# Kernel tuning notes

Hardware: AMD Instinct MI355X
Metric: run time of the kernel (lower is better)

Reference implementation:

```python
import jax, jax.numpy as jnp
import numpy as np

B, L, N, DOUT = 8, 8192, 256, 256  # batch, seq_len, state_dim, output_dim


def setup_inputs() -> dict:
    key = jax.random.key(0)
    k_u, k_h, k_w = jax.random.split(key, 3)
    u = jax.random.normal(k_u, (B, L, 1), dtype=jnp.float32)
    # impulse response buffer (stands in for A_bar^i @ B_bar rows); decay-scaled for realism
    h = jax.random.normal(k_h, (L, N), dtype=jnp.float32) * 0.02
    W = jax.random.normal(k_w, (DOUT, N), dtype=jnp.float32) * (1.0 / np.sqrt(N))
    return {"u": u, "h": h, "W": W}


def reference(u, h, W):
    L_ = h.shape[0]
    n_fft = 2 * L_
    # FFT-based long convolution: U:[B, n_fft//2+1, 1], H:[n_fft//2+1, N]
    U = jnp.fft.rfft(u, n=n_fft, axis=1)
    H = jnp.fft.rfft(h, n=n_fft, axis=0)
    M = U * H[None, :, :]                      # broadcast channel 1 -> N
    m = jnp.fft.irfft(M, n=n_fft, axis=1)[:, :L_, :]  # [B, L, N]
    return jnp.einsum('bln,on->blo', m, W)     # Linear(state_dim -> output_dim), no bias
```

## Files before the change

### kernel.cpp

```cpp
#include <hip/hip_runtime.h>
#include <hip/hip_bf16.h>
#include <stdint.h>
#include <stddef.h>

typedef __attribute__((ext_vector_type(4))) float f32x4;
typedef __attribute__((ext_vector_type(8))) short s16x8;

#define B_    8
#define L_    8192
#define N_    256
#define DOUT_ 256
#define M_    8192
#define GSTRIDE 8200
#define RC    0.70710678118654752f

__device__ __forceinline__ unsigned short f2bf(float f) {
  unsigned int x = __float_as_uint(f);
  x += 0x7fff + ((x >> 16) & 1);
  return (unsigned short)(x >> 16);
}

__device__ __forceinline__ float2 cmul(float2 a, float2 b) {
  return make_float2(a.x * b.x - a.y * b.y, a.x * b.y + a.y * b.x);
}
__device__ __forceinline__ float2 cadd(float2 a, float2 b) { return make_float2(a.x + b.x, a.y + b.y); }
__device__ __forceinline__ float2 csub(float2 a, float2 b) { return make_float2(a.x - b.x, a.y - b.y); }

__device__ __forceinline__ int phi(int i) { return i ^ (((i >> 4) ^ (i >> 7)) & 15); }
__device__ __forceinline__ int rev13(int i) { return (int)(__brev((unsigned)i) >> 19); }

template<bool INV> __device__ __forceinline__ float2 twmul(float2 x, float2 w) {
  return INV ? make_float2(x.x * w.x + x.y * w.y, x.y * w.x - x.x * w.y)
             : make_float2(x.x * w.x - x.y * w.y, x.x * w.y + x.y * w.x);
}
template<bool INV> __device__ __forceinline__ float2 mul_mi(float2 x) {
  return INV ? make_float2(-x.y, x.x) : make_float2(x.y, -x.x);
}
template<bool INV> __device__ __forceinline__ float2 mul_w8(float2 x) {
  return INV ? make_float2(RC * (x.x - x.y), RC * (x.x + x.y))
             : make_float2(RC * (x.x + x.y), RC * (x.y - x.x));
}
template<bool INV> __device__ __forceinline__ float2 mul_w83(float2 x) {
  return INV ? make_float2(-RC * (x.x + x.y), RC * (x.x - x.y))
             : make_float2(RC * (x.y - x.x), -RC * (x.x + x.y));
}

__global__ void k_tw(float2* __restrict__ tw) {
  int k = blockIdx.x * 256 + threadIdx.x;
  float a = (float)k * 3.8349519697141029e-4f;
  tw[k] = make_float2(__cosf(a), -__sinf(a));
}

__global__ void k_gt(const float* __restrict__ W, const float* __restrict__ h,
                     unsigned short* __restrict__ gT) {
  int gid  = blockIdx.x * 256 + threadIdx.x;
  int lane = gid & 63;
  int wid  = gid >> 6;
  int o_t  = wid >> 7;
  int i_t  = wid & 127;
  int o0 = o_t * 16, i0 = i_t * 64;
  int ln = lane & 15, hi = lane >> 4;
  f32x4 acc[4] = {};
#pragma unroll
  for (int k0 = 0; k0 < N_; k0 += 32) {
    const float* wp = W + (o0 + ln) * N_ + k0 + 8 * hi;
    float4 w0 = *(const float4*)wp;
    float4 w1 = *(const float4*)(wp + 4);
    s16x8 a;
    a[0] = (short)f2bf(w0.x); a[1] = (short)f2bf(w0.y);
    a[2] = (short)f2bf(w0.z); a[3] = (short)f2bf(w0.w);
    a[4] = (short)f2bf(w1.x); a[5] = (short)f2bf(w1.y);
    a[6] = (short)f2bf(w1.z); a[7] = (short)f2bf(w1.w);
#pragma unroll
    for (int ns = 0; ns < 4; ++ns) {
      const float* hp = h + (size_t)(i0 + 16 * ns + ln) * N_ + k0 + 8 * hi;
      float4 h0 = *(const float4*)hp;
      float4 h1 = *(const float4*)(hp + 4);
      s16x8 bb;
      bb[0] = (short)f2bf(h0.x); bb[1] = (short)f2bf(h0.y);
      bb[2] = (short)f2bf(h0.z); bb[3] = (short)f2bf(h0.w);
      bb[4] = (short)f2bf(h1.x); bb[5] = (short)f2bf(h1.y);
      bb[6] = (short)f2bf(h1.z); bb[7] = (short)f2bf(h1.w);
      acc[ns] = __builtin_amdgcn_mfma_f32_16x16x32_bf16(a, bb, acc[ns], 0, 0, 0);
    }
  }
#pragma unroll
  for (int ns = 0; ns < 4; ++ns)
#pragma unroll
    for (int q = 0; q < 4; ++q)
      gT[(size_t)(o0 + 4 * hi + q) * L_ + i0 + 16 * ns + ln] = f2bf(acc[ns][q]);
}

template<bool INV>
__device__ __forceinline__ void fft13(float2* zc, const float2* __restrict__ tw, int tid) {
#pragma unroll
  for (int s = 0; s <= 6; s += 3) {
    const int shQ = 10 - s;
    const int Q = 1 << shQ;
#pragma unroll
    for (int it = 0; it < 2; ++it) {
      int j = tid + 512 * it;
      int g = j >> shQ;
      int p = j & (Q - 1);
      int base = (g << (shQ + 3)) + p;
      int ix[8];
      float2 a[8];
#pragma unroll
      for (int k = 0; k < 8; ++k) ix[k] = phi(base + (k << shQ));
#pragma unroll
      for (int k = 0; k < 8; ++k) a[k] = zc[ix[k]];
      float2 w1 = tw[p << (s + 1)];
      float2 w2 = tw[p << (s + 2)];
      float2 w4 = tw[p << (s + 3)];
      float2 b[8];
#pragma unroll
      for (int k = 0; k < 4; ++k) {
        b[k] = cadd(a[k], a[k + 4]);
        float2 t = twmul<INV>(csub(a[k], a[k + 4]), w1);
        if (k == 1) t = mul_w8<INV>(t);
        else if (k == 2) t = mul_mi<INV>(t);
        else if (k == 3) t = mul_w83<INV>(t);
        b[k + 4] = t;
      }
      float2 c[8];
#pragma unroll
      for (int blk = 0; blk < 8; blk += 4)
#pragma unroll
        for (int k = 0; k < 2; ++k) {
          c[blk + k] = cadd(b[blk + k], b[blk + k + 2]);
          float2 t = twmul<INV>(csub(b[blk + k], b[blk + k + 2]), w2);
          if (k == 1) t = mul_mi<INV>(t);
          c[blk + k + 2] = t;
        }
#pragma unroll
      for (int blk = 0; blk < 8; blk += 2) {
        zc[ix[blk]]     = cadd(c[blk], c[blk + 1]);
        zc[ix[blk + 1]] = twmul<INV>(csub(c[blk], c[blk + 1]), w4);
      }
    }
    __syncthreads();
  }
  {
    const int base = tid << 4;
    int ix[16];
    float2 a[16];
#pragma unroll
    for (int k = 0; k < 16; ++k) ix[k] = phi(base + k);
#pragma unroll
    for (int k = 0; k < 16; ++k) a[k] = zc[ix[k]];
    float2 b[16];
#pragma unroll
    for (int k = 0; k < 8; ++k) {
      b[k] = cadd(a[k], a[k + 8]);
      float2 t = csub(a[k], a[k + 8]);
      if (k) t = twmul<INV>(t, tw[k << 10]);
      b[k + 8] = t;
    }
    float2 c[16];
#pragma unroll
    for (int blk = 0; blk < 16; blk += 8)
#pragma unroll
      for (int k = 0; k < 4; ++k) {
        c[blk + k] = cadd(b[blk + k], b[blk + k + 4]);
        float2 t = csub(b[blk + k], b[blk + k + 4]);
        if (k == 1) t = mul_w8<INV>(t);
        else if (k == 2) t = mul_mi<INV>(t);
        else if (k == 3) t = mul_w83<INV>(t);
        c[blk + k + 4] = t;
      }
    float2 d[16];
#pragma unroll
    for (int blk = 0; blk < 16; blk += 4) {
      d[blk]     = cadd(c[blk], c[blk + 2]);
      d[blk + 2] = csub(c[blk], c[blk + 2]);
      d[blk + 1] = cadd(c[blk + 1], c[blk + 3]);
      d[blk + 3] = mul_mi<INV>(csub(c[blk + 1], c[blk + 3]));
    }
#pragma unroll
    for (int blk = 0; blk < 16; blk += 2) {
      zc[ix[blk]]     = cadd(d[blk], d[blk + 1]);
      zc[ix[blk + 1]] = csub(d[blk], d[blk + 1]);
    }
  }
  __syncthreads();
}

__global__ __launch_bounds__(512, 4) void k_ffwd(const float* __restrict__ u,
                                                 const unsigned short* __restrict__ gT,
                                                 const float2* __restrict__ tw,
                                                 float2* __restrict__ U,
                                                 float2* __restrict__ G) {
  __shared__ float2 zc[M_];
  const int wg = blockIdx.x;
  const int tid = threadIdx.x;

  if (wg < 8) {
    const float2* src = (const float2*)(u + wg * L_);
#pragma unroll 4
    for (int kp = 0; kp < 16; ++kp) {
      int t = tid + 512 * kp;
      zc[phi(t)] = (t < 4096) ? src[t] : make_float2(0.f, 0.f);
    }
  } else {
    const unsigned int* src = (const unsigned int*)(gT + (size_t)(wg - 8) * L_);
#pragma unroll 4
    for (int kp = 0; kp < 16; ++kp) {
      int t = tid + 512 * kp;
      float2 v = make_float2(0.f, 0.f);
      if (t < 4096) {
        unsigned int pr = src[t];
        v.x = __uint_as_float(pr << 16);
        v.y = __uint_as_float(pr & 0xffff0000u);
      }
      zc[phi(t)] = v;
    }
  }
  __syncthreads();

  fft13<false>(zc, tw, tid);

  float2* dst = (wg < 8) ? (U + (size_t)wg * GSTRIDE) : (G + (size_t)(wg - 8) * GSTRIDE);
#pragma unroll 4
  for (int kp = 0; kp < 16; ++kp) {
    int k = tid + 512 * kp;
    float2 zk  = zc[phi(rev13(k))];
    float2 zmk = zc[phi(rev13((M_ - k) & (M_ - 1)))];
    float2 E = make_float2(0.5f * (zk.x + zmk.x), 0.5f * (zk.y - zmk.y));
    float2 O = make_float2(0.5f * (zk.y + zmk.y), 0.5f * (zmk.x - zk.x));
    float2 w = tw[k];
    float2 X = cmul(w, O);
    dst[k] = make_float2(E.x + X.x, E.y + X.y);
  }
  if (tid == 0) {
    float2 z0 = zc[0];
    dst[M_] = make_float2(z0.x - z0.y, 0.f);
  }
}

__global__ __launch_bounds__(512, 4) void k_conv(const float2* __restrict__ U,
                                                 const float2* __restrict__ G,
                                                 const float2* __restrict__ tw,
                                                 float* __restrict__ out) {
  __shared__ float2 zc[M_];
  const int bid = blockIdx.x;
  const int widx = (bid & 7) * 256 + (bid >> 3);
  const int b = widx >> 8;
  const int o = widx & 255;
  const int tid = threadIdx.x;
  const float2* Ub = U + (size_t)b * GSTRIDE;
  const float2* Go = G + (size_t)o * GSTRIDE;

#pragma unroll 4
  for (int kp = 0; kp < 16; ++kp) {
    int k = tid + 512 * kp;
    float2 Yk  = cmul(Ub[k], Go[k]);
    float2 Ymk = cmul(Ub[M_ - k], Go[M_ - k]);
    float2 E = make_float2(0.5f * (Yk.x + Ymk.x), 0.5f * (Yk.y - Ymk.y));
    float2 D = make_float2(0.5f * (Yk.x - Ymk.x), 0.5f * (Yk.y + Ymk.y));
    float2 w = tw[k];
    float2 O = make_float2(D.x * w.x + D.y * w.y, -D.x * w.y + D.y * w.x);
    zc[phi(k)] = make_float2(E.x - O.y, E.y + O.x);
  }
  __syncthreads();

  fft13<true>(zc, tw, tid);

  const float s1 = 1.0f / 8192.0f;
  float* ob = out + (size_t)b * (L_ * DOUT_) + o;
#pragma unroll 2
  for (int kp = 0; kp < 8; ++kp) {
    int t = tid + 512 * kp;
    float2 z = zc[phi(rev13(t))];
    ob[(size_t)(2 * t) * DOUT_]     = z.x * s1;
    ob[(size_t)(2 * t + 1) * DOUT_] = z.y * s1;
  }
}

extern "C" void kernel_launch(void* const* d_in, const int* in_sizes, int n_in,
                              void* d_out, int out_size, void* d_ws, size_t ws_size,
                              hipStream_t stream) {
  const float* u = (const float*)d_in[0];
  const float* h = (const float*)d_in[1];
  const float* W = (const float*)d_in[2];
  float* out = (float*)d_out;

  char* ws = (char*)d_ws;
  unsigned short* gT = (unsigned short*)ws;
  float2* tw = (float2*)(ws + (size_t)4 * 1024 * 1024);
  float2* U  = (float2*)(ws + (size_t)4 * 1024 * 1024 + 65536);
  float2* G  = (float2*)(ws + (size_t)4 * 1024 * 1024 + 65536 + 524800);

  k_tw<<<32, 256, 0, stream>>>(tw);
  k_gt<<<512, 256, 0, stream>>>(W, h, gT);
  k_ffwd<<<264, 512, 0, stream>>>(u, gT, tw, U, G);
  k_conv<<<2048, 512, 0, stream>>>(U, G, tw, out);
}
```

Before: 188.5 us.

## Restructure 8192-point FFT as three radix-16 passes plus fused final radix-2

Replaces the radix-8×3 plus radix-16 FFT (four LDS passes) with three radix-16 passes over 12 bits. The last radix-2 stage is folded into the post-processing reads, which fetch adjacent pairs with float4 LDS loads. Twiddles are preloaded into registers, the bank swizzle is changed to keep pairs contiguous, and the inverse pre-processing exploits Hermitian symmetry to compute both k and M-k per iteration. The aim is to cut LDS round trips, syncthreads and global twiddle loads, at the cost of more register pressure from the 16-point butterflies and 12 held twiddles.

```diff
diff --git a/kernel.cpp b/kernel.cpp
--- a/kernel.cpp
+++ b/kernel.cpp
@@ -13,6 +13,8 @@
 #define M_    8192
 #define GSTRIDE 8200
 #define RC    0.70710678118654752f
+#define C8    0.92387953251128675613f
+#define S8    0.38268343236508977173f
 
 __device__ __forceinline__ unsigned short f2bf(float f) {
   unsigned int x = __float_as_uint(f);
@@ -26,7 +28,9 @@
 __device__ __forceinline__ float2 cadd(float2 a, float2 b) { return make_float2(a.x + b.x, a.y + b.y); }
 __device__ __forceinline__ float2 csub(float2 a, float2 b) { return make_float2(a.x - b.x, a.y - b.y); }
 
-__device__ __forceinline__ int phi(int i) { return i ^ (((i >> 4) ^ (i >> 7)) & 15); }
+__device__ __forceinline__ int phi(int i) {
+  return i ^ ((((i >> 4) ^ (i >> 7) ^ (i >> 10)) & 7) << 1);
+}
 __device__ __forceinline__ int rev13(int i) { return (int)(__brev((unsigned)i) >> 19); }
 
 template<bool INV> __device__ __forceinline__ float2 twmul(float2 x, float2 w) {
@@ -43,6 +47,78 @@
 template<bool INV> __device__ __forceinline__ float2 mul_w83(float2 x) {
   return INV ? make_float2(-RC * (x.x + x.y), RC * (x.x - x.y))
              : make_float2(RC * (x.y - x.x), -RC * (x.x + x.y));
+}
+
+template<bool INV>
+__device__ __forceinline__ void r16(float2* a, float2 wA, float2 wB, float2 wC, float2 wD) {
+  float2 b[16];
+#pragma unroll
+  for (int k = 0; k < 8; ++k) {
+    b[k] = cadd(a[k], a[k + 8]);
+    float2 t = twmul<INV>(csub(a[k], a[k + 8]), wA);
+    if (k == 1) t = twmul<INV>(t, make_float2(C8, -S8));
+    else if (k == 2) t = mul_w8<INV>(t);
+    else if (k == 3) t = twmul<INV>(t, make_float2(S8, -C8));
+    else if (k == 4) t = mul_mi<INV>(t);
+    else if (k == 5) t = twmul<INV>(t, make_float2(-S8, -C8));
+    else if (k == 6) t = mul_w83<INV>(t);
+    else if (k == 7) t = twmul<INV>(t, make_float2(-C8, -S8));
+    b[k + 8] = t;
+  }
+  float2 c[16];
+#pragma unroll
+  for (int blk = 0; blk < 16; blk += 8)
+#pragma unroll
+    for (int k = 0; k < 4; ++k) {
+      c[blk + k] = cadd(b[blk + k], b[blk + k + 4]);
+      float2 t = twmul<INV>(csub(b[blk + k], b[blk + k + 4]), wB);
+      if (k == 1) t = mul_w8<INV>(t);
+      else if (k == 2) t = mul_mi<INV>(t);
+      else if (k == 3) t = mul_w83<INV>(t);
+      c[blk + k + 4] = t;
+    }
+  float2 d[16];
+#pragma unroll
+  for (int blk = 0; blk < 16; blk += 4)
+#pragma unroll
+    for (int k = 0; k < 2; ++k) {
+      d[blk + k] = cadd(c[blk + k], c[blk + k + 2]);
+      float2 t = twmul<INV>(csub(c[blk + k], c[blk + k + 2]), wC);
+      if (k == 1) t = mul_mi<INV>(t);
+      d[blk + k + 2] = t;
+    }
+#pragma unroll
+  for (int blk = 0; blk < 16; blk += 2) {
+    a[blk]     = cadd(d[blk], d[blk + 1]);
+    a[blk + 1] = twmul<INV>(csub(d[blk], d[blk + 1]), wD);
+  }
+}
+
+__device__ __forceinline__ void preload_tw(const float2* __restrict__ tw, int tid, float2* twp) {
+  const int p0 = tid, p1 = tid & 31, p2 = tid & 1;
+  twp[0] = tw[p0 << 1];  twp[1] = tw[p0 << 2];  twp[2]  = tw[p0 << 3];  twp[3]  = tw[p0 << 4];
+  twp[4] = tw[p1 << 5];  twp[5] = tw[p1 << 6];  twp[6]  = tw[p1 << 7];  twp[7]  = tw[p1 << 8];
+  twp[8] = tw[p2 << 9];  twp[9] = tw[p2 << 10]; twp[10] = tw[p2 << 11]; twp[11] = tw[p2 << 12];
+}
+
+#define FFT_PASS(INV, SH, BASE, W0, W1, W2, W3) do { \
+    const int base_ = (BASE); \
+    float2 a_[16]; \
+    _Pragma("unroll") \
+    for (int k = 0; k < 16; ++k) a_[k] = zc[phi(base_ + (k << (SH)))]; \
+    r16<INV>(a_, W0, W1, W2, W3); \
+    _Pragma("unroll") \
+    for (int k = 0; k < 16; ++k) zc[phi(base_ + (k << (SH)))] = a_[k]; \
+  } while (0)
+
+template<bool INV>
+__device__ __forceinline__ void fft12(float2* zc, int tid, const float2* twp) {
+  FFT_PASS(INV, 9, tid, twp[0], twp[1], twp[2], twp[3]);
+  __syncthreads();
+  FFT_PASS(INV, 5, ((tid >> 5) << 9) + (tid & 31), twp[4], twp[5], twp[6], twp[7]);
+  __syncthreads();
+  FFT_PASS(INV, 1, ((tid >> 1) << 5) + (tid & 1), twp[8], twp[9], twp[10], twp[11]);
+  __syncthreads();
 }
 
 __global__ void k_tw(float2* __restrict__ tw) {
@@ -91,108 +167,16 @@
       gT[(size_t)(o0 + 4 * hi + q) * L_ + i0 + 16 * ns + ln] = f2bf(acc[ns][q]);
 }
 
-template<bool INV>
-__device__ __forceinline__ void fft13(float2* zc, const float2* __restrict__ tw, int tid) {
-#pragma unroll
-  for (int s = 0; s <= 6; s += 3) {
-    const int shQ = 10 - s;
-    const int Q = 1 << shQ;
-#pragma unroll
-    for (int it = 0; it < 2; ++it) {
-      int j = tid + 512 * it;
-      int g = j >> shQ;
-      int p = j & (Q - 1);
-      int base = (g << (shQ + 3)) + p;
-      int ix[8];
-      float2 a[8];
-#pragma unroll
-      for (int k = 0; k < 8; ++k) ix[k] = phi(base + (k << shQ));
-#pragma unroll
-      for (int k = 0; k < 8; ++k) a[k] = zc[ix[k]];
-      float2 w1 = tw[p << (s + 1)];
-      float2 w2 = tw[p << (s + 2)];
-      float2 w4 = tw[p << (s + 3)];
-      float2 b[8];
-#pragma unroll
-      for (int k = 0; k < 4; ++k) {
-        b[k] = cadd(a[k], a[k + 4]);
-        float2 t = twmul<INV>(csub(a[k], a[k + 4]), w1);
-        if (k == 1) t = mul_w8<INV>(t);
-        else if (k == 2) t = mul_mi<INV>(t);
-        else if (k == 3) t = mul_w83<INV>(t);
-        b[k + 4] = t;
-      }
-      float2 c[8];
-#pragma unroll
-      for (int blk = 0; blk < 8; blk += 4)
-#pragma unroll
-        for (int k = 0; k < 2; ++k) {
-          c[blk + k] = cadd(b[blk + k], b[blk + k + 2]);
-          float2 t = twmul<INV>(csub(b[blk + k], b[blk + k + 2]), w2);
-          if (k == 1) t = mul_mi<INV>(t);
-          c[blk + k + 2] = t;
-        }
-#pragma unroll
-      for (int blk = 0; blk < 8; blk += 2) {
-        zc[ix[blk]]     = cadd(c[blk], c[blk + 1]);
-        zc[ix[blk + 1]] = twmul<INV>(csub(c[blk], c[blk + 1]), w4);
-      }
-    }
-    __syncthreads();
-  }
-  {
-    const int base = tid << 4;
-    int ix[16];
-    float2 a[16];
-#pragma unroll
-    for (int k = 0; k < 16; ++k) ix[k] = phi(base + k);
-#pragma unroll
-    for (int k = 0; k < 16; ++k) a[k] = zc[ix[k]];
-    float2 b[16];
-#pragma unroll
-    for (int k = 0; k < 8; ++k) {
-      b[k] = cadd(a[k], a[k + 8]);
-      float2 t = csub(a[k], a[k + 8]);
-      if (k) t = twmul<INV>(t, tw[k << 10]);
-      b[k + 8] = t;
-    }
-    float2 c[16];
-#pragma unroll
-    for (int blk = 0; blk < 16; blk += 8)
-#pragma unroll
-      for (int k = 0; k < 4; ++k) {
-        c[blk + k] = cadd(b[blk + k], b[blk + k + 4]);
-        float2 t = csub(b[blk + k], b[blk + k + 4]);
-        if (k == 1) t = mul_w8<INV>(t);
-        else if (k == 2) t = mul_mi<INV>(t);
-        else if (k == 3) t = mul_w83<INV>(t);
-        c[blk + k + 4] = t;
-      }
-    float2 d[16];
-#pragma unroll
-    for (int blk = 0; blk < 16; blk += 4) {
-      d[blk]     = cadd(c[blk], c[blk + 2]);
-      d[blk + 2] = csub(c[blk], c[blk + 2]);
-      d[blk + 1] = cadd(c[blk + 1], c[blk + 3]);
-      d[blk + 3] = mul_mi<INV>(csub(c[blk + 1], c[blk + 3]));
-    }
-#pragma unroll
-    for (int blk = 0; blk < 16; blk += 2) {
-      zc[ix[blk]]     = cadd(d[blk], d[blk + 1]);
-      zc[ix[blk + 1]] = csub(d[blk], d[blk + 1]);
-    }
-  }
-  __syncthreads();
-}
-
 __global__ __launch_bounds__(512, 4) void k_ffwd(const float* __restrict__ u,
                                                  const unsigned short* __restrict__ gT,
                                                  const float2* __restrict__ tw,
                                                  float2* __restrict__ U,
                                                  float2* __restrict__ G) {
-  __shared__ float2 zc[M_];
+  __shared__ __align__(16) float2 zc[M_];
   const int wg = blockIdx.x;
   const int tid = threadIdx.x;
+  float2 twp[12];
+  preload_tw(tw, tid, twp);
 
   if (wg < 8) {
     const float2* src = (const float2*)(u + wg * L_);
@@ -217,14 +201,20 @@
   }
   __syncthreads();
 
-  fft13<false>(zc, tw, tid);
+  fft12<false>(zc, tid, twp);
 
   float2* dst = (wg < 8) ? (U + (size_t)wg * GSTRIDE) : (G + (size_t)(wg - 8) * GSTRIDE);
 #pragma unroll 4
   for (int kp = 0; kp < 16; ++kp) {
     int k = tid + 512 * kp;
-    float2 zk  = zc[phi(rev13(k))];
-    float2 zmk = zc[phi(rev13((M_ - k) & (M_ - 1)))];
+    int m1 = rev13(k);
+    int m2 = rev13((M_ - k) & (M_ - 1));
+    float4 v1 = *(const float4*)(zc + phi(m1 & ~1));
+    float4 v2 = *(const float4*)(zc + phi(m2 & ~1));
+    float2 zk  = (m1 & 1) ? make_float2(v1.x - v1.z, v1.y - v1.w)
+                          : make_float2(v1.x + v1.z, v1.y + v1.w);
+    float2 zmk = (m2 & 1) ? make_float2(v2.x - v2.z, v2.y - v2.w)
+                          : make_float2(v2.x + v2.z, v2.y + v2.w);
     float2 E = make_float2(0.5f * (zk.x + zmk.x), 0.5f * (zk.y - zmk.y));
     float2 O = make_float2(0.5f * (zk.y + zmk.y), 0.5f * (zmk.x - zk.x));
     float2 w = tw[k];
@@ -232,7 +222,8 @@
     dst[k] = make_float2(E.x + X.x, E.y + X.y);
   }
   if (tid == 0) {
-    float2 z0 = zc[0];
+    float4 v = *(const float4*)zc;
+    float2 z0 = make_float2(v.x + v.z, v.y + v.w);
     dst[M_] = make_float2(z0.x - z0.y, 0.f);
   }
 }
@@ -241,7 +232,7 @@
                                                  const float2* __restrict__ G,
                                                  const float2* __restrict__ tw,
                                                  float* __restrict__ out) {
-  __shared__ float2 zc[M_];
+  __shared__ __align__(16) float2 zc[M_];
   const int bid = blockIdx.x;
   const int widx = (bid & 7) * 256 + (bid >> 3);
   const int b = widx >> 8;
@@ -249,30 +240,43 @@
   const int tid = threadIdx.x;
   const float2* Ub = U + (size_t)b * GSTRIDE;
   const float2* Go = G + (size_t)o * GSTRIDE;
-
-#pragma unroll 4
-  for (int kp = 0; kp < 16; ++kp) {
+  float2 twp[12];
+  preload_tw(tw, tid, twp);
+
+#pragma unroll 2
+  for (int kp = 0; kp < 8; ++kp) {
     int k = tid + 512 * kp;
-    float2 Yk  = cmul(Ub[k], Go[k]);
-    float2 Ymk = cmul(Ub[M_ - k], Go[M_ - k]);
-    float2 E = make_float2(0.5f * (Yk.x + Ymk.x), 0.5f * (Yk.y - Ymk.y));
-    float2 D = make_float2(0.5f * (Yk.x - Ymk.x), 0.5f * (Yk.y + Ymk.y));
-    float2 w = tw[k];
-    float2 O = make_float2(D.x * w.x + D.y * w.y, -D.x * w.y + D.y * w.x);
-    zc[phi(k)] = make_float2(E.x - O.y, E.y + O.x);
-  }
-  __syncthreads();
-
-  fft13<true>(zc, tw, tid);
+    float2 Yk = cmul(Ub[k], Go[k]);
+    if (k == 0) {
+      float2 Ym = cmul(Ub[M_], Go[M_]);
+      float2 E = make_float2(0.5f * (Yk.x + Ym.x), 0.5f * (Yk.y - Ym.y));
+      float2 D = make_float2(0.5f * (Yk.x - Ym.x), 0.5f * (Yk.y + Ym.y));
+      zc[0] = make_float2(E.x - D.y, E.y + D.x);
+      float2 Y4 = cmul(Ub[4096], Go[4096]);
+      zc[phi(4096)] = make_float2(Y4.x, -Y4.y);
+    } else {
+      float2 Ymk = cmul(Ub[M_ - k], Go[M_ - k]);
+      float2 E = make_float2(0.5f * (Yk.x + Ymk.x), 0.5f * (Yk.y - Ymk.y));
+      float2 D = make_float2(0.5f * (Yk.x - Ymk.x), 0.5f * (Yk.y + Ymk.y));
+      float2 w = tw[k];
+      float2 O = make_float2(D.x * w.x + D.y * w.y, -D.x * w.y + D.y * w.x);
+      zc[phi(k)]      = make_float2(E.x - O.y,  E.y + O.x);
+      zc[phi(M_ - k)] = make_float2(E.x + O.y, -E.y + O.x);
+    }
+  }
+  __syncthreads();
+
+  fft12<true>(zc, tid, twp);
 
   const float s1 = 1.0f / 8192.0f;
   float* ob = out + (size_t)b * (L_ * DOUT_) + o;
 #pragma unroll 2
   for (int kp = 0; kp < 8; ++kp) {
     int t = tid + 512 * kp;
-    float2 z = zc[phi(rev13(t))];
-    ob[(size_t)(2 * t) * DOUT_]     = z.x * s1;
-    ob[(size_t)(2 * t + 1) * DOUT_] = z.y * s1;
+    int m = rev13(t);
+    float4 v = *(const float4*)(zc + phi(m));
+    ob[(size_t)(2 * t) * DOUT_]     = (v.x + v.z) * s1;
+    ob[(size_t)(2 * t + 1) * DOUT_] = (v.y + v.w) * s1;
   }
 }
 
```

Measured after the change: 187.5 us. No clear change (-0.5%).
